# Optimization experiments

Hardware: AMD Instinct MI355X
Metric: run time of the kernel (lower is better)

## Reference

```python
import jax, jax.numpy as jnp
import numpy as np

HEADS = 16
DIM_HEAD = 64
SCALE = float(np.sqrt(DIM_HEAD))  # NOTE: original code MULTIPLIES by sqrt(dim_head)


def setup_inputs() -> dict:
    key = jax.random.key(0)
    k1, k2, k3, k4 = jax.random.split(key, 4)
    dim = 1024
    b, n = 2, 2048
    s = 1.0 / np.sqrt(dim)
    return {
        "x": jax.random.normal(k1, (b, n, dim), dtype=jnp.float32),
        "w_q": jax.random.normal(k2, (dim, HEADS * DIM_HEAD), dtype=jnp.float32) * s,
        "w_vk": jax.random.normal(k3, (dim, HEADS * DIM_HEAD * 2), dtype=jnp.float32) * s,
        "w_out": jax.random.normal(k4, (HEADS * DIM_HEAD, dim), dtype=jnp.float32) * s,
    }


def reference(x, w_q, w_vk, w_out):
    b, n, _ = x.shape
    h, d = HEADS, DIM_HEAD
    context = x  # context=None, kv_include_self=False
    q = (x @ w_q).reshape(b, n, h, d).transpose(0, 2, 1, 3)          # b h n d
    kv = context @ w_vk                                              # b n 2hd
    k, v = jnp.split(kv, 2, axis=-1)                                 # chunk order: k first, v second
    k = k.reshape(b, n, h, d).transpose(0, 2, 1, 3)
    v = v.reshape(b, n, h, d).transpose(0, 2, 1, 3)
    dots = jnp.einsum('bhid,bhjd->bhij', q, k) * SCALE               # faithful: multiply by sqrt(d)
    attn = jax.nn.softmax(dots, axis=-1)                             # dropout p=0 -> identity
    out = jnp.einsum('bhij,bhjd->bhid', attn, v)
    out = out.transpose(0, 2, 1, 3).reshape(b, n, h * d)
    return out @ w_out
```

## Files before the change

kernel.cpp:

```cpp
#include <hip/hip_runtime.h>

typedef _Float16 half4 __attribute__((ext_vector_type(4)));
typedef _Float16 half8 __attribute__((ext_vector_type(8)));
typedef float f32x4 __attribute__((ext_vector_type(4)));

#define MFMA_F16K32(a, b, c) __builtin_amdgcn_mfma_f32_16x16x32_f16(a, b, c, 0, 0, 0)
#define MFMA_F16K16(a, b, c) __builtin_amdgcn_mfma_f32_16x16x16f16(a, b, c, 0, 0, 0)
#define EXP2F(x) __builtin_amdgcn_exp2f(x)

constexpr int NSEQ = 2048, DIM = 1024;
constexpr int MROWS = 4096;
constexpr float QSCALE = 11.5415603271f;

__device__ __forceinline__ void ld_lds16(void* lds, const void* g) {
  __builtin_amdgcn_global_load_lds(
      (const __attribute__((address_space(1))) void*)g,
      (__attribute__((address_space(3))) void*)lds, 16, 0, 0);
}

__global__ __launch_bounds__(256) void prep(
    const float* __restrict__ w_q, const float* __restrict__ w_vk,
    const float* __restrict__ w_out, const float* __restrict__ x,
    _Float16* __restrict__ WT, _Float16* __restrict__ WoT,
    _Float16* __restrict__ xf) {
  const int bid = blockIdx.x;
  const int t = threadIdx.x;
  if (bid >= 1024) {
    const size_t i = ((size_t)(bid - 1024) * 256 + t) * 8;
    float4 a = *(const float4*)(x + i), b2 = *(const float4*)(x + i + 4);
    float v[8] = {a.x, a.y, a.z, a.w, b2.x, b2.y, b2.z, b2.w};
    half8 h;
#pragma unroll
    for (int j = 0; j < 8; ++j) h[j] = (_Float16)v[j];
    *(half8*)(xf + i) = h;
    return;
  }
  __shared__ float T[64][65];
  const int bx = bid & 63, k0 = (bid >> 6) * 64;
  const float* src;
  int srcN, n0, dstrow, mode;
  float scale;
  if (bx < 16) {
    src = w_q; srcN = 1024; n0 = bx * 64; dstrow = n0; scale = QSCALE; mode = 0;
  } else if (bx < 48) {
    src = w_vk; srcN = 2048; n0 = (bx - 16) * 64; dstrow = 1024 + n0;
    scale = 1.0f; mode = 0;
  } else {
    src = w_out; srcN = 1024; n0 = (bx - 48) * 64; dstrow = n0;
    scale = 1.0f; mode = 1;
  }
  {
    const int r = t >> 2, c4 = (t & 3) * 16;
    const float* s = src + (size_t)(k0 + r) * srcN + n0 + c4;
    float4 v0 = ((const float4*)s)[0], v1 = ((const float4*)s)[1],
           v2 = ((const float4*)s)[2], v3 = ((const float4*)s)[3];
    *(float4*)&T[r][c4 + 0] = v0;  *(float4*)&T[r][c4 + 4] = v1;
    *(float4*)&T[r][c4 + 8] = v2;  *(float4*)&T[r][c4 + 12] = v3;
  }
  __syncthreads();
  const int rn = t >> 2, kc = (t & 3) * 16;
  half8 hv[2];
#pragma unroll
  for (int half = 0; half < 2; ++half)
#pragma unroll
    for (int j = 0; j < 8; ++j)
      hv[half][j] = (_Float16)(T[kc + half * 8 + j][rn] * scale);
  _Float16* d = ((mode == 0) ? WT + (size_t)(dstrow + rn) * 1024
                             : WoT + (size_t)(n0 + rn) * 1024) + k0 + kc;
  *(half8*)d = hv[0]; *(half8*)(d + 8) = hv[1];
}

__global__ __launch_bounds__(256, 3) void proj6(
    const _Float16* __restrict__ xf, const _Float16* __restrict__ WT,
    _Float16* __restrict__ qb, _Float16* __restrict__ kb,
    _Float16* __restrict__ VT) {
  __shared__ __align__(16) char smem[32768];
  const int t = threadIdx.x;
  const int lane = t & 63, wave = t >> 6, quad = lane >> 4, lq = lane & 15;
  const int bn = blockIdx.x * 128, bm = blockIdx.y * 128;
  const int kind = bn >> 10;
  const int wm = (wave >> 1) * 64, wn = (wave & 1) * 64;

  const int srow = lane >> 2;
  const int schk = (lane & 3) ^ (srow & 3);
  const _Float16* xg = xf + (size_t)(bm + wave * 32 + srow) * DIM + schk * 8;
  const _Float16* bg = WT + (size_t)(bn + wave * 32 + srow) * DIM + schk * 8;
  const int wb = wave * 2048;

  auto issue = [&](char* buf, int k0) {
    ld_lds16(buf + wb,                xg + k0);
    ld_lds16(buf + wb + 1024,         xg + k0 + 16 * DIM);
    ld_lds16(buf + 8192 + wb,         bg + k0);
    ld_lds16(buf + 8192 + wb + 1024,  bg + k0 + 16 * DIM);
  };

  const int swz = (quad ^ (lq & 3)) * 8;

  f32x4 acc[4][4];
#pragma unroll
  for (int i = 0; i < 4; ++i)
#pragma unroll
    for (int j = 0; j < 4; ++j) acc[i][j] = (f32x4){0.f, 0.f, 0.f, 0.f};

  char* bufA = smem;
  char* bufB = smem + 16384;
  issue(bufA, 0);
  for (int k0 = 0; k0 < DIM; k0 += 32) {
    char* cur = ((k0 >> 5) & 1) ? bufB : bufA;
    char* nxt = ((k0 >> 5) & 1) ? bufA : bufB;
    __syncthreads();
    if (k0 + 32 < DIM) issue(nxt, k0 + 32);
    const _Float16* Xs = (const _Float16*)cur;
    const _Float16* Bs = (const _Float16*)(cur + 8192);
    half8 ah[4];
#pragma unroll
    for (int i = 0; i < 4; ++i)
      ah[i] = *(const half8*)&Xs[(wm + i * 16 + lq) * 32 + swz];
#pragma unroll
    for (int j = 0; j < 4; ++j) {
      half8 bf = *(const half8*)&Bs[(wn + j * 16 + lq) * 32 + swz];
#pragma unroll
      for (int i = 0; i < 4; ++i) acc[i][j] = MFMA_F16K32(ah[i], bf, acc[i][j]);
    }
  }

  if (kind == 2) {
#pragma unroll
    for (int i = 0; i < 4; ++i)
#pragma unroll
      for (int j = 0; j < 4; ++j) {
        const int c = (bn - 2048) + wn + j * 16 + lq;
        const int row0 = bm + wm + i * 16 + quad * 4;
        const int b = row0 >> 11, n = row0 & 2047;
        const int h = c >> 6, d = c & 63;
        half4 o;
#pragma unroll
        for (int r = 0; r < 4; ++r) o[r] = (_Float16)acc[i][j][r];
        *(half4*)(VT + ((size_t)(b * 16 + h) * 64 + d) * 2048 + n) = o;
      }
  } else {
    _Float16* D = (kind == 0) ? qb : kb;
    const int cb = bn & 1023;
#pragma unroll
    for (int i = 0; i < 4; ++i)
#pragma unroll
      for (int j = 0; j < 4; ++j) {
        const int col = cb + wn + j * 16 + lq;
#pragma unroll
        for (int r = 0; r < 4; ++r) {
          const int row = bm + wm + i * 16 + quad * 4 + r;
          D[(size_t)row * 1024 + col] = (_Float16)acc[i][j][r];
        }
      }
  }
}

__global__ __launch_bounds__(256, 2) void attn7(
    const _Float16* __restrict__ qb, const _Float16* __restrict__ kb,
    const _Float16* __restrict__ vT, _Float16* __restrict__ ho) {
  __shared__ __align__(16) char smem[65536];
  const int t = threadIdx.x;
  const int lane = t & 63, wave = t >> 6, quad = lane >> 4, lq = lane & 15;
  const int i0 = blockIdx.x * 128;
  const int bh = blockIdx.y, b = bh >> 4, head = bh & 15;
  const size_t rowbase = (size_t)b * NSEQ;

  half8 qf[2][2];
#pragma unroll
  for (int qt = 0; qt < 2; ++qt) {
    const _Float16* qp =
        qb + (rowbase + i0 + wave * 32 + qt * 16 + lq) * DIM + head * 64 + quad * 8;
    qf[qt][0] = *(const half8*)qp;
    qf[qt][1] = *(const half8*)(qp + 32);
  }

  f32x4 o[2][4];
#pragma unroll
  for (int qt = 0; qt < 2; ++qt)
#pragma unroll
    for (int dt = 0; dt < 4; ++dt) o[qt][dt] = (f32x4){0.f, 0.f, 0.f, 0.f};
  float mrun[2] = {-3.0e38f, -3.0e38f};
  float lrun[2] = {0.f, 0.f};

  const int srow = lane >> 3, schk = (lane & 7) ^ srow;
  const _Float16* kg =
      kb + (rowbase + wave * 32 + srow) * DIM + head * 64 + schk * 8;
  int vco[4];
#pragma unroll
  for (int is = 0; is < 4; ++is)
    vco[is] = ((lane & 15) ^ (is * 4 + (lane >> 4))) * 8;
  const _Float16* vg = vT + ((size_t)bh * 64 + wave * 16 + (lane >> 4)) * NSEQ;

  auto issue = [&](char* buf, int j0) {
#pragma unroll
    for (int is = 0; is < 4; ++is) {
      ld_lds16(buf + wave * 4096 + is * 1024,
               kg + ((size_t)j0 + is * 8) * DIM);
      ld_lds16(buf + 16384 + (wave * 16 + is * 4) * 256,
               vg + (size_t)is * 4 * NSEQ + j0 + vco[is]);
    }
  };

  const int swzK0 = (quad ^ (lq & 7)) * 8;
  const int swzK1 = ((quad + 4) ^ (lq & 7)) * 8;

  char* bufA = smem;
  char* bufB = smem + 32768;
  issue(bufA, 0);

  for (int j0 = 0; j0 < NSEQ; j0 += 128) {
    char* cur = ((j0 >> 7) & 1) ? bufB : bufA;
    char* nxt = ((j0 >> 7) & 1) ? bufA : bufB;
    __syncthreads();
    if (j0 + 128 < NSEQ) issue(nxt, j0 + 128);
    const _Float16* Khs = (const _Float16*)cur;
    const _Float16* Vts = (const _Float16*)(cur + 16384);

#pragma unroll
    for (int jh = 0; jh < 2; ++jh) {
      f32x4 s[2][4];
#pragma unroll
      for (int nt = 0; nt < 4; ++nt) {
        const int roff = (jh * 64 + nt * 16 + lq) * 64;
        half8 k0f = *(const half8*)&Khs[roff + swzK0];
        half8 k1f = *(const half8*)&Khs[roff + swzK1];
#pragma unroll
        for (int qt = 0; qt < 2; ++qt) {
          f32x4 sv = (f32x4){0.f, 0.f, 0.f, 0.f};
          sv = MFMA_F16K32(k0f, qf[qt][0], sv);
          sv = MFMA_F16K32(k1f, qf[qt][1], sv);
          s[qt][nt] = sv;
        }
      }
      half4 pb[2][4];
#pragma unroll
      for (int qt = 0; qt < 2; ++qt) {
        float mx = s[qt][0][0];
#pragma unroll
        for (int nt = 0; nt < 4; ++nt)
#pragma unroll
          for (int r = 0; r < 4; ++r) mx = fmaxf(mx, s[qt][nt][r]);
        mx = fmaxf(mx, __shfl_xor(mx, 16));
        mx = fmaxf(mx, __shfl_xor(mx, 32));
        const float mn = fmaxf(mrun[qt], mx);
        const float alpha = EXP2F(mrun[qt] - mn);
        mrun[qt] = mn;
        float rs = 0.f;
#pragma unroll
        for (int nt = 0; nt < 4; ++nt)
#pragma unroll
          for (int r = 0; r < 4; ++r) {
            float p = EXP2F(s[qt][nt][r] - mn);
            rs += p;
            pb[qt][nt][r] = (_Float16)p;
          }
        rs += __shfl_xor(rs, 16);
        rs += __shfl_xor(rs, 32);
        lrun[qt] = lrun[qt] * alpha + rs;
#pragma unroll
        for (int dt = 0; dt < 4; ++dt) o[qt][dt] *= alpha;
      }
#pragma unroll
      for (int dt = 0; dt < 4; ++dt) {
        const int vrow = (dt * 16 + lq) * 128;
#pragma unroll
        for (int nt = 0; nt < 4; ++nt) {
          const int ntj = jh * 4 + nt;
          const int voff =
              vrow + ((2 * ntj + (quad >> 1)) ^ lq) * 8 + (quad & 1) * 4;
          half4 va = *(const half4*)&Vts[voff];
          o[0][dt] = MFMA_F16K16(va, pb[0][nt], o[0][dt]);
          o[1][dt] = MFMA_F16K16(va, pb[1][nt], o[1][dt]);
        }
      }
    }
  }

  _Float16* Ots = (_Float16*)smem;
  __syncthreads();
#pragma unroll
  for (int qt = 0; qt < 2; ++qt) {
    const float inv = 1.0f / lrun[qt];
#pragma unroll
    for (int dt = 0; dt < 4; ++dt)
#pragma unroll
      for (int r = 0; r < 4; ++r)
        Ots[(wave * 32 + qt * 16 + lq) * 80 + dt * 16 + quad * 4 + r] =
            (_Float16)(o[qt][dt][r] * inv);
  }
  __syncthreads();
  {
    const int row = t >> 1, hf = t & 1;
    const _Float16* src = &Ots[row * 80 + hf * 32];
    half8 o0 = ((const half8*)src)[0], o1 = ((const half8*)src)[1],
          o2 = ((const half8*)src)[2], o3 = ((const half8*)src)[3];
    _Float16* dst = ho + (rowbase + i0 + row) * DIM + head * 64 + hf * 32;
    ((half8*)dst)[0] = o0; ((half8*)dst)[1] = o1;
    ((half8*)dst)[2] = o2; ((half8*)dst)[3] = o3;
  }
}

__global__ __launch_bounds__(256, 4) void gemm_out(
    const _Float16* __restrict__ A, const _Float16* __restrict__ BT,
    float* __restrict__ C) {
  __shared__ __align__(16) char smem[24576];
  const int t = threadIdx.x;
  const int lane = t & 63, wave = t >> 6, quad = lane >> 4, lq = lane & 15;
  const int bn = blockIdx.x * 128, bm = blockIdx.y * 64;
  const int wm = (wave >> 1) * 32, wn = (wave & 1) * 64;

  const int bco = (lane & 7) ^ (lane >> 3);
  const int brow = 2 * (lane >> 3) + (bco >> 2);
  const int bcc = bco & 3;
  const _Float16* ag = A + (size_t)(bm + wave * 16 + brow) * DIM + bcc * 8;
  const _Float16* bg = BT + (size_t)(bn + wave * 32 + brow) * DIM + bcc * 8;
  const int swzB = ((((lq & 1) << 2) | quad) ^ ((lq >> 1) & 7)) * 8;

  auto issue = [&](char* buf, int k0) {
    ld_lds16(buf + wave * 1024,               ag + k0);
    ld_lds16(buf + 4096 + wave * 2048,        bg + k0);
    ld_lds16(buf + 4096 + wave * 2048 + 1024, bg + k0 + 16 * DIM);
  };

  f32x4 acc[2][4];
#pragma unroll
  for (int i = 0; i < 2; ++i)
#pragma unroll
    for (int j = 0; j < 4; ++j) acc[i][j] = (f32x4){0.f, 0.f, 0.f, 0.f};

  char* bufA = smem;
  char* bufB = smem + 12288;
  issue(bufA, 0);
  for (int k0 = 0; k0 < DIM; k0 += 32) {
    char* cur = ((k0 >> 5) & 1) ? bufB : bufA;
    char* nxt = ((k0 >> 5) & 1) ? bufA : bufB;
    __syncthreads();
    if (k0 + 32 < DIM) issue(nxt, k0 + 32);
    const _Float16* Ahs = (const _Float16*)cur;
    const _Float16* Bhs = (const _Float16*)(cur + 4096);
    half8 ah[2];
#pragma unroll
    for (int i = 0; i < 2; ++i) {
      const int row = wm + i * 16 + lq;
      ah[i] = *(const half8*)&Ahs[(row >> 1) * 64 + swzB];
    }
#pragma unroll
    for (int j = 0; j < 4; ++j) {
      const int row = wn + j * 16 + lq;
      half8 bf = *(const half8*)&Bhs[(row >> 1) * 64 + swzB];
#pragma unroll
      for (int i = 0; i < 2; ++i) acc[i][j] = MFMA_F16K32(ah[i], bf, acc[i][j]);
    }
  }
#pragma unroll
  for (int i = 0; i < 2; ++i)
#pragma unroll
    for (int j = 0; j < 4; ++j) {
      const int col = bn + wn + j * 16 + lq;
#pragma unroll
      for (int r = 0; r < 4; ++r) {
        const int row = bm + wm + i * 16 + quad * 4 + r;
        C[(size_t)row * 1024 + col] = acc[i][j][r];
      }
    }
}

extern "C" void kernel_launch(void* const* d_in, const int* in_sizes, int n_in,
                              void* d_out, int out_size, void* d_ws,
                              size_t ws_size, hipStream_t stream) {
  const float* x     = (const float*)d_in[0];
  const float* w_q   = (const float*)d_in[1];
  const float* w_vk  = (const float*)d_in[2];
  const float* w_out = (const float*)d_in[3];
  float* out = (float*)d_out;

  char* w = (char*)d_ws;
  _Float16* wT  = (_Float16*)(w);
  _Float16* woT = (_Float16*)(w + (6ull << 20));
  _Float16* qbb = (_Float16*)(w + (8ull << 20));
  _Float16* kbb = (_Float16*)(w + (16ull << 20));
  _Float16* vTb = (_Float16*)(w + (24ull << 20));
  _Float16* hob = (_Float16*)(w + (32ull << 20));
  _Float16* xfb = (_Float16*)(w + (40ull << 20));

  dim3 blk(256);
  prep<<<dim3(3072), blk, 0, stream>>>(w_q, w_vk, w_out, x, wT, woT, xfb);
  proj6<<<dim3(24, 32), blk, 0, stream>>>(xfb, wT, qbb, kbb, vTb);
  attn7<<<dim3(16, 32), blk, 0, stream>>>(qbb, kbb, vTb, hob);
  gemm_out<<<dim3(8, 64), blk, 0, stream>>>(hob, woT, out);
}
```

Measured before the change: 187.5 us.

## Split attention block across eight waves of sixteen query rows each

The attention kernel now runs 512-thread blocks, so each of eight waves owns 16 query rows instead of four waves owning 32. The K/V tile loads are redistributed across the waves with a matching V swizzle, and the output write-back is spread over all 512 threads. Each wave now handles the full 128-key tile in one pass instead of two 64-key halves. Probabilities are converted with packed fp16 conversion, and MFMA sections are wrapped in s_setprio. The aim is more waves to hide latency and less per-wave softmax bookkeeping, but the (512,4) launch bound sharply caps VGPRs per thread and may cause spills, while 64KB LDS per block still limits how many blocks fit on a CU.

```diff
diff --git a/kernel.cpp b/kernel.cpp
--- a/kernel.cpp
+++ b/kernel.cpp
@@ -2,11 +2,13 @@
 
 typedef _Float16 half4 __attribute__((ext_vector_type(4)));
 typedef _Float16 half8 __attribute__((ext_vector_type(8)));
+typedef _Float16 h2pk __attribute__((ext_vector_type(2)));
 typedef float f32x4 __attribute__((ext_vector_type(4)));
 
 #define MFMA_F16K32(a, b, c) __builtin_amdgcn_mfma_f32_16x16x32_f16(a, b, c, 0, 0, 0)
 #define MFMA_F16K16(a, b, c) __builtin_amdgcn_mfma_f32_16x16x16f16(a, b, c, 0, 0, 0)
 #define EXP2F(x) __builtin_amdgcn_exp2f(x)
+#define CVT_PK(a, b) __builtin_bit_cast(h2pk, __builtin_amdgcn_cvt_pkrtz(a, b))
 
 constexpr int NSEQ = 2048, DIM = 1024;
 constexpr int MROWS = 4096;
@@ -155,7 +157,7 @@
   }
 }
 
-__global__ __launch_bounds__(256, 2) void attn7(
+__global__ __launch_bounds__(512, 4) void attn7(
     const _Float16* __restrict__ qb, const _Float16* __restrict__ kb,
     const _Float16* __restrict__ vT, _Float16* __restrict__ ho) {
   __shared__ __align__(16) char smem[65536];
@@ -165,38 +167,36 @@
   const int bh = blockIdx.y, b = bh >> 4, head = bh & 15;
   const size_t rowbase = (size_t)b * NSEQ;
 
-  half8 qf[2][2];
-#pragma unroll
-  for (int qt = 0; qt < 2; ++qt) {
+  half8 qf0, qf1;
+  {
     const _Float16* qp =
-        qb + (rowbase + i0 + wave * 32 + qt * 16 + lq) * DIM + head * 64 + quad * 8;
-    qf[qt][0] = *(const half8*)qp;
-    qf[qt][1] = *(const half8*)(qp + 32);
-  }
-
-  f32x4 o[2][4];
-#pragma unroll
-  for (int qt = 0; qt < 2; ++qt)
-#pragma unroll
-    for (int dt = 0; dt < 4; ++dt) o[qt][dt] = (f32x4){0.f, 0.f, 0.f, 0.f};
-  float mrun[2] = {-3.0e38f, -3.0e38f};
-  float lrun[2] = {0.f, 0.f};
+        qb + (rowbase + i0 + wave * 16 + lq) * DIM + head * 64 + quad * 8;
+    qf0 = *(const half8*)qp;
+    qf1 = *(const half8*)(qp + 32);
+  }
+
+  f32x4 o[4];
+#pragma unroll
+  for (int dt = 0; dt < 4; ++dt) o[dt] = (f32x4){0.f, 0.f, 0.f, 0.f};
+  float mrun = -3.0e38f;
+  float lrun = 0.f;
 
   const int srow = lane >> 3, schk = (lane & 7) ^ srow;
   const _Float16* kg =
-      kb + (rowbase + wave * 32 + srow) * DIM + head * 64 + schk * 8;
-  int vco[4];
-#pragma unroll
-  for (int is = 0; is < 4; ++is)
-    vco[is] = ((lane & 15) ^ (is * 4 + (lane >> 4))) * 8;
-  const _Float16* vg = vT + ((size_t)bh * 64 + wave * 16 + (lane >> 4)) * NSEQ;
+      kb + (rowbase + wave * 16 + srow) * DIM + head * 64 + schk * 8;
+  const int vr = lane >> 4;
+  int vco[2];
+#pragma unroll
+  for (int is = 0; is < 2; ++is)
+    vco[is] = ((lane & 15) ^ ((wave & 1) * 8 + is * 4 + vr)) * 8;
+  const _Float16* vg = vT + ((size_t)bh * 64 + wave * 8 + vr) * NSEQ;
 
   auto issue = [&](char* buf, int j0) {
 #pragma unroll
-    for (int is = 0; is < 4; ++is) {
-      ld_lds16(buf + wave * 4096 + is * 1024,
+    for (int is = 0; is < 2; ++is) {
+      ld_lds16(buf + wave * 2048 + is * 1024,
                kg + ((size_t)j0 + is * 8) * DIM);
-      ld_lds16(buf + 16384 + (wave * 16 + is * 4) * 256,
+      ld_lds16(buf + 16384 + (wave * 8 + is * 4) * 256,
                vg + (size_t)is * 4 * NSEQ + j0 + vco[is]);
     }
   };
@@ -216,87 +216,88 @@
     const _Float16* Khs = (const _Float16*)cur;
     const _Float16* Vts = (const _Float16*)(cur + 16384);
 
-#pragma unroll
-    for (int jh = 0; jh < 2; ++jh) {
-      f32x4 s[2][4];
-#pragma unroll
-      for (int nt = 0; nt < 4; ++nt) {
-        const int roff = (jh * 64 + nt * 16 + lq) * 64;
-        half8 k0f = *(const half8*)&Khs[roff + swzK0];
-        half8 k1f = *(const half8*)&Khs[roff + swzK1];
-#pragma unroll
-        for (int qt = 0; qt < 2; ++qt) {
-          f32x4 sv = (f32x4){0.f, 0.f, 0.f, 0.f};
-          sv = MFMA_F16K32(k0f, qf[qt][0], sv);
-          sv = MFMA_F16K32(k1f, qf[qt][1], sv);
-          s[qt][nt] = sv;
-        }
+    f32x4 s[8];
+    __builtin_amdgcn_s_setprio(1);
+#pragma unroll
+    for (int nt = 0; nt < 8; ++nt) {
+      const int roff = (nt * 16 + lq) * 64;
+      half8 k0f = *(const half8*)&Khs[roff + swzK0];
+      half8 k1f = *(const half8*)&Khs[roff + swzK1];
+      f32x4 sv = (f32x4){0.f, 0.f, 0.f, 0.f};
+      sv = MFMA_F16K32(k0f, qf0, sv);
+      sv = MFMA_F16K32(k1f, qf1, sv);
+      s[nt] = sv;
+    }
+    __builtin_amdgcn_s_setprio(0);
+
+    float mx;
+    {
+      float m0 = fmaxf(fmaxf(s[0][0], s[0][1]), fmaxf(s[0][2], s[0][3]));
+      float m1 = fmaxf(fmaxf(s[1][0], s[1][1]), fmaxf(s[1][2], s[1][3]));
+      float m2 = fmaxf(fmaxf(s[2][0], s[2][1]), fmaxf(s[2][2], s[2][3]));
+      float m3 = fmaxf(fmaxf(s[3][0], s[3][1]), fmaxf(s[3][2], s[3][3]));
+      float m4 = fmaxf(fmaxf(s[4][0], s[4][1]), fmaxf(s[4][2], s[4][3]));
+      float m5 = fmaxf(fmaxf(s[5][0], s[5][1]), fmaxf(s[5][2], s[5][3]));
+      float m6 = fmaxf(fmaxf(s[6][0], s[6][1]), fmaxf(s[6][2], s[6][3]));
+      float m7 = fmaxf(fmaxf(s[7][0], s[7][1]), fmaxf(s[7][2], s[7][3]));
+      mx = fmaxf(fmaxf(fmaxf(m0, m1), fmaxf(m2, m3)),
+                 fmaxf(fmaxf(m4, m5), fmaxf(m6, m7)));
+    }
+    mx = fmaxf(mx, __shfl_xor(mx, 16));
+    mx = fmaxf(mx, __shfl_xor(mx, 32));
+    const float mn = fmaxf(mrun, mx);
+    const float alpha = EXP2F(mrun - mn);
+    mrun = mn;
+    float rs = 0.f;
+    half4 pb[8];
+#pragma unroll
+    for (int nt = 0; nt < 8; ++nt) {
+      float p0 = EXP2F(s[nt][0] - mn), p1 = EXP2F(s[nt][1] - mn);
+      float p2 = EXP2F(s[nt][2] - mn), p3 = EXP2F(s[nt][3] - mn);
+      rs += (p0 + p1) + (p2 + p3);
+      h2pk lo = CVT_PK(p0, p1);
+      h2pk hi = CVT_PK(p2, p3);
+      pb[nt] = (half4){lo[0], lo[1], hi[0], hi[1]};
+    }
+    rs += __shfl_xor(rs, 16);
+    rs += __shfl_xor(rs, 32);
+    lrun = lrun * alpha + rs;
+#pragma unroll
+    for (int dt = 0; dt < 4; ++dt) o[dt] *= alpha;
+
+    __builtin_amdgcn_s_setprio(1);
+#pragma unroll
+    for (int dt = 0; dt < 4; ++dt) {
+      const int vrow = (dt * 16 + lq) * 128;
+#pragma unroll
+      for (int ntj = 0; ntj < 8; ++ntj) {
+        const int voff =
+            vrow + ((2 * ntj + (quad >> 1)) ^ lq) * 8 + (quad & 1) * 4;
+        half4 va = *(const half4*)&Vts[voff];
+        o[dt] = MFMA_F16K16(va, pb[ntj], o[dt]);
       }
-      half4 pb[2][4];
-#pragma unroll
-      for (int qt = 0; qt < 2; ++qt) {
-        float mx = s[qt][0][0];
-#pragma unroll
-        for (int nt = 0; nt < 4; ++nt)
-#pragma unroll
-          for (int r = 0; r < 4; ++r) mx = fmaxf(mx, s[qt][nt][r]);
-        mx = fmaxf(mx, __shfl_xor(mx, 16));
-        mx = fmaxf(mx, __shfl_xor(mx, 32));
-        const float mn = fmaxf(mrun[qt], mx);
-        const float alpha = EXP2F(mrun[qt] - mn);
-        mrun[qt] = mn;
-        float rs = 0.f;
-#pragma unroll
-        for (int nt = 0; nt < 4; ++nt)
-#pragma unroll
-          for (int r = 0; r < 4; ++r) {
-            float p = EXP2F(s[qt][nt][r] - mn);
-            rs += p;
-            pb[qt][nt][r] = (_Float16)p;
-          }
-        rs += __shfl_xor(rs, 16);
-        rs += __shfl_xor(rs, 32);
-        lrun[qt] = lrun[qt] * alpha + rs;
-#pragma unroll
-        for (int dt = 0; dt < 4; ++dt) o[qt][dt] *= alpha;
-      }
-#pragma unroll
-      for (int dt = 0; dt < 4; ++dt) {
-        const int vrow = (dt * 16 + lq) * 128;
-#pragma unroll
-        for (int nt = 0; nt < 4; ++nt) {
-          const int ntj = jh * 4 + nt;
-          const int voff =
-              vrow + ((2 * ntj + (quad >> 1)) ^ lq) * 8 + (quad & 1) * 4;
-          half4 va = *(const half4*)&Vts[voff];
-          o[0][dt] = MFMA_F16K16(va, pb[0][nt], o[0][dt]);
-          o[1][dt] = MFMA_F16K16(va, pb[1][nt], o[1][dt]);
-        }
-      }
-    }
+    }
+    __builtin_amdgcn_s_setprio(0);
   }
 
   _Float16* Ots = (_Float16*)smem;
   __syncthreads();
-#pragma unroll
-  for (int qt = 0; qt < 2; ++qt) {
-    const float inv = 1.0f / lrun[qt];
+  {
+    const float inv = 1.0f / lrun;
 #pragma unroll
     for (int dt = 0; dt < 4; ++dt)
 #pragma unroll
       for (int r = 0; r < 4; ++r)
-        Ots[(wave * 32 + qt * 16 + lq) * 80 + dt * 16 + quad * 4 + r] =
-            (_Float16)(o[qt][dt][r] * inv);
+        Ots[(wave * 16 + lq) * 80 + dt * 16 + quad * 4 + r] =
+            (_Float16)(o[dt][r] * inv);
   }
   __syncthreads();
   {
-    const int row = t >> 1, hf = t & 1;
-    const _Float16* src = &Ots[row * 80 + hf * 32];
-    half8 o0 = ((const half8*)src)[0], o1 = ((const half8*)src)[1],
-          o2 = ((const half8*)src)[2], o3 = ((const half8*)src)[3];
-    _Float16* dst = ho + (rowbase + i0 + row) * DIM + head * 64 + hf * 32;
+    const int row = t >> 2, seg = t & 3;
+    const _Float16* src = &Ots[row * 80 + seg * 16];
+    half8 o0 = ((const half8*)src)[0], o1 = ((const half8*)src)[1];
+    _Float16* dst = ho + (rowbase + i0 + row) * DIM + head * 64 + seg * 16;
     ((half8*)dst)[0] = o0; ((half8*)dst)[1] = o1;
-    ((half8*)dst)[2] = o2; ((half8*)dst)[3] = o3;
   }
 }
 
@@ -386,6 +387,6 @@
   dim3 blk(256);
   prep<<<dim3(3072), blk, 0, stream>>>(w_q, w_vk, w_out, x, wT, woT, xfb);
   proj6<<<dim3(24, 32), blk, 0, stream>>>(xfb, wT, qbb, kbb, vTb);
-  attn7<<<dim3(16, 32), blk, 0, stream>>>(qbb, kbb, vTb, hob);
+  attn7<<<dim3(16, 32), dim3(512), 0, stream>>>(qbb, kbb, vTb, hob);
   gemm_out<<<dim3(8, 64), blk, 0, stream>>>(hob, woT, out);
 }
```

After: 192.1 us. 2.4% more time.

## Split attention KV sequence across two wave groups and merge partial softmax states

Applied to the files above, without the earlier changes.

The attention kernel now uses 512 threads per block in two groups of four waves. Each group handles alternating 64-key tiles of the same 128 query rows, and at the end group 1 dumps its partial O, max and sum to LDS for group 0 to merge. The aim is more waves per CU for latency hiding and MFMA/exp overlap; it also adds s_setprio around the MFMA sections and packed f16 conversion. The costs are a final merge pass, per-wave register pressure under launch_bounds(512,4), and smaller per-group tiles.

```diff
diff --git a/kernel.cpp b/kernel.cpp
--- a/kernel.cpp
+++ b/kernel.cpp
@@ -2,14 +2,15 @@
 
 typedef _Float16 half4 __attribute__((ext_vector_type(4)));
 typedef _Float16 half8 __attribute__((ext_vector_type(8)));
+typedef _Float16 h2pk __attribute__((ext_vector_type(2)));
 typedef float f32x4 __attribute__((ext_vector_type(4)));
 
 #define MFMA_F16K32(a, b, c) __builtin_amdgcn_mfma_f32_16x16x32_f16(a, b, c, 0, 0, 0)
 #define MFMA_F16K16(a, b, c) __builtin_amdgcn_mfma_f32_16x16x16f16(a, b, c, 0, 0, 0)
 #define EXP2F(x) __builtin_amdgcn_exp2f(x)
+#define CVT_PK(a, b) __builtin_bit_cast(h2pk, __builtin_amdgcn_cvt_pkrtz(a, b))
 
 constexpr int NSEQ = 2048, DIM = 1024;
-constexpr int MROWS = 4096;
 constexpr float QSCALE = 11.5415603271f;
 
 __device__ __forceinline__ void ld_lds16(void* lds, const void* g) {
@@ -155,12 +156,13 @@
   }
 }
 
-__global__ __launch_bounds__(256, 2) void attn7(
+__global__ __launch_bounds__(512, 4) void attn8(
     const _Float16* __restrict__ qb, const _Float16* __restrict__ kb,
     const _Float16* __restrict__ vT, _Float16* __restrict__ ho) {
   __shared__ __align__(16) char smem[65536];
   const int t = threadIdx.x;
   const int lane = t & 63, wave = t >> 6, quad = lane >> 4, lq = lane & 15;
+  const int group = wave >> 2, wq = wave & 3;
   const int i0 = blockIdx.x * 128;
   const int bh = blockIdx.y, b = bh >> 4, head = bh & 15;
   const size_t rowbase = (size_t)b * NSEQ;
@@ -169,7 +171,7 @@
 #pragma unroll
   for (int qt = 0; qt < 2; ++qt) {
     const _Float16* qp =
-        qb + (rowbase + i0 + wave * 32 + qt * 16 + lq) * DIM + head * 64 + quad * 8;
+        qb + (rowbase + i0 + wq * 32 + qt * 16 + lq) * DIM + head * 64 + quad * 8;
     qf[qt][0] = *(const half8*)qp;
     qf[qt][1] = *(const half8*)(qp + 32);
   }
@@ -183,120 +185,140 @@
   float lrun[2] = {0.f, 0.f};
 
   const int srow = lane >> 3, schk = (lane & 7) ^ srow;
-  const _Float16* kg =
-      kb + (rowbase + wave * 32 + srow) * DIM + head * 64 + schk * 8;
-  int vco[4];
-#pragma unroll
-  for (int is = 0; is < 4; ++is)
-    vco[is] = ((lane & 15) ^ (is * 4 + (lane >> 4))) * 8;
-  const _Float16* vg = vT + ((size_t)bh * 64 + wave * 16 + (lane >> 4)) * NSEQ;
-
-  auto issue = [&](char* buf, int j0) {
-#pragma unroll
-    for (int is = 0; is < 4; ++is) {
-      ld_lds16(buf + wave * 4096 + is * 1024,
-               kg + ((size_t)j0 + is * 8) * DIM);
-      ld_lds16(buf + 16384 + (wave * 16 + is * 4) * 256,
-               vg + (size_t)is * 4 * NSEQ + j0 + vco[is]);
-    }
+  const _Float16* kgp =
+      kb + (rowbase + wq * 16 + srow) * DIM + head * 64 + schk * 8;
+  const _Float16* vgp =
+      vT + ((size_t)bh * 64 + wq * 16 + srow) * 2048 + schk * 8;
+
+  auto issue = [&](int bsel, int j) {
+    char* kd = smem + (group * 2 + bsel) * 8192 + wq * 2048;
+    char* vd = kd + 32768;
+    ld_lds16(kd,        kgp + (size_t)j * DIM);
+    ld_lds16(kd + 1024, kgp + (size_t)(j + 8) * DIM);
+    ld_lds16(vd,        vgp + j);
+    ld_lds16(vd + 1024, vgp + 8 * 2048 + j);
   };
 
   const int swzK0 = (quad ^ (lq & 7)) * 8;
   const int swzK1 = ((quad + 4) ^ (lq & 7)) * 8;
 
-  char* bufA = smem;
-  char* bufB = smem + 32768;
-  issue(bufA, 0);
-
-  for (int j0 = 0; j0 < NSEQ; j0 += 128) {
-    char* cur = ((j0 >> 7) & 1) ? bufB : bufA;
-    char* nxt = ((j0 >> 7) & 1) ? bufA : bufB;
+  issue(0, group * 64);
+
+  for (int p = 0; p < 16; ++p) {
+    const int cur = p & 1;
     __syncthreads();
-    if (j0 + 128 < NSEQ) issue(nxt, j0 + 128);
-    const _Float16* Khs = (const _Float16*)cur;
-    const _Float16* Vts = (const _Float16*)(cur + 16384);
-
-#pragma unroll
-    for (int jh = 0; jh < 2; ++jh) {
-      f32x4 s[2][4];
+    if (p < 15) issue(cur ^ 1, (2 * p + group) * 64 + 128);
+    const _Float16* Khs = (const _Float16*)(smem + (group * 2 + cur) * 8192);
+    const _Float16* Vts = (const _Float16*)(smem + 32768 + (group * 2 + cur) * 8192);
+
+    f32x4 s[2][4];
+    __builtin_amdgcn_s_setprio(1);
+#pragma unroll
+    for (int nt = 0; nt < 4; ++nt) {
+      const int roff = (nt * 16 + lq) * 64;
+      half8 k0f = *(const half8*)&Khs[roff + swzK0];
+      half8 k1f = *(const half8*)&Khs[roff + swzK1];
+#pragma unroll
+      for (int qt = 0; qt < 2; ++qt) {
+        f32x4 sv = (f32x4){0.f, 0.f, 0.f, 0.f};
+        sv = MFMA_F16K32(k0f, qf[qt][0], sv);
+        sv = MFMA_F16K32(k1f, qf[qt][1], sv);
+        s[qt][nt] = sv;
+      }
+    }
+    __builtin_amdgcn_s_setprio(0);
+
+    half4 pbv[2][4];
+#pragma unroll
+    for (int qt = 0; qt < 2; ++qt) {
+      float m0 = fmaxf(fmaxf(s[qt][0][0], s[qt][0][1]),
+                       fmaxf(s[qt][0][2], s[qt][0][3]));
+      float m1 = fmaxf(fmaxf(s[qt][1][0], s[qt][1][1]),
+                       fmaxf(s[qt][1][2], s[qt][1][3]));
+      float m2 = fmaxf(fmaxf(s[qt][2][0], s[qt][2][1]),
+                       fmaxf(s[qt][2][2], s[qt][2][3]));
+      float m3 = fmaxf(fmaxf(s[qt][3][0], s[qt][3][1]),
+                       fmaxf(s[qt][3][2], s[qt][3][3]));
+      float mx = fmaxf(fmaxf(m0, m1), fmaxf(m2, m3));
+      mx = fmaxf(mx, __shfl_xor(mx, 16));
+      mx = fmaxf(mx, __shfl_xor(mx, 32));
+      const float mn = fmaxf(mrun[qt], mx);
+      const float alpha = EXP2F(mrun[qt] - mn);
+      mrun[qt] = mn;
+      float rs = 0.f;
 #pragma unroll
       for (int nt = 0; nt < 4; ++nt) {
-        const int roff = (jh * 64 + nt * 16 + lq) * 64;
-        half8 k0f = *(const half8*)&Khs[roff + swzK0];
-        half8 k1f = *(const half8*)&Khs[roff + swzK1];
-#pragma unroll
-        for (int qt = 0; qt < 2; ++qt) {
-          f32x4 sv = (f32x4){0.f, 0.f, 0.f, 0.f};
-          sv = MFMA_F16K32(k0f, qf[qt][0], sv);
-          sv = MFMA_F16K32(k1f, qf[qt][1], sv);
-          s[qt][nt] = sv;
+        float p0 = EXP2F(s[qt][nt][0] - mn), p1 = EXP2F(s[qt][nt][1] - mn);
+        float p2 = EXP2F(s[qt][nt][2] - mn), p3 = EXP2F(s[qt][nt][3] - mn);
+        rs += (p0 + p1) + (p2 + p3);
+        h2pk lo = CVT_PK(p0, p1);
+        h2pk hi = CVT_PK(p2, p3);
+        pbv[qt][nt] = (half4){lo[0], lo[1], hi[0], hi[1]};
+      }
+      rs += __shfl_xor(rs, 16);
+      rs += __shfl_xor(rs, 32);
+      lrun[qt] = lrun[qt] * alpha + rs;
+#pragma unroll
+      for (int dt = 0; dt < 4; ++dt) o[qt][dt] *= alpha;
+    }
+
+    __builtin_amdgcn_s_setprio(1);
+#pragma unroll
+    for (int dt = 0; dt < 4; ++dt) {
+      const int vrow = (dt * 16 + lq) * 64;
+#pragma unroll
+      for (int ntj = 0; ntj < 4; ++ntj) {
+        const int voff =
+            vrow + (((2 * ntj + (quad >> 1)) ^ (lq & 7)) * 8) + (quad & 1) * 4;
+        half4 va = *(const half4*)&Vts[voff];
+        o[0][dt] = MFMA_F16K16(va, pbv[0][ntj], o[0][dt]);
+        o[1][dt] = MFMA_F16K16(va, pbv[1][ntj], o[1][dt]);
+      }
+    }
+    __builtin_amdgcn_s_setprio(0);
+  }
+
+  float* dump = (float*)smem;
+  __syncthreads();
+  if (group == 1) {
+    float* D = dump + wq * 2304 + lane * 36;
+#pragma unroll
+    for (int qt = 0; qt < 2; ++qt)
+#pragma unroll
+      for (int dt = 0; dt < 4; ++dt)
+        *(f32x4*)(D + (qt * 4 + dt) * 4) = o[qt][dt];
+    D[32] = mrun[0]; D[33] = lrun[0]; D[34] = mrun[1]; D[35] = lrun[1];
+  }
+  __syncthreads();
+  _Float16* Ots = (_Float16*)(smem + 40960);
+  if (group == 0) {
+    const float* D = dump + wq * 2304 + lane * 36;
+#pragma unroll
+    for (int qt = 0; qt < 2; ++qt) {
+      const float m2 = D[32 + qt * 2], l2 = D[33 + qt * 2];
+      const float mM = fmaxf(mrun[qt], m2);
+      const float f1 = EXP2F(mrun[qt] - mM);
+      const float f2 = EXP2F(m2 - mM);
+      const float inv = 1.0f / (lrun[qt] * f1 + l2 * f2);
+#pragma unroll
+      for (int dt = 0; dt < 4; ++dt) {
+        f32x4 o2 = *(const f32x4*)(D + (qt * 4 + dt) * 4);
+#pragma unroll
+        for (int r = 0; r < 4; ++r) {
+          const float val = (o[qt][dt][r] * f1 + o2[r] * f2) * inv;
+          Ots[(wq * 32 + qt * 16 + lq) * 80 + dt * 16 + quad * 4 + r] =
+              (_Float16)val;
         }
       }
-      half4 pb[2][4];
-#pragma unroll
-      for (int qt = 0; qt < 2; ++qt) {
-        float mx = s[qt][0][0];
-#pragma unroll
-        for (int nt = 0; nt < 4; ++nt)
-#pragma unroll
-          for (int r = 0; r < 4; ++r) mx = fmaxf(mx, s[qt][nt][r]);
-        mx = fmaxf(mx, __shfl_xor(mx, 16));
-        mx = fmaxf(mx, __shfl_xor(mx, 32));
-        const float mn = fmaxf(mrun[qt], mx);
-        const float alpha = EXP2F(mrun[qt] - mn);
-        mrun[qt] = mn;
-        float rs = 0.f;
-#pragma unroll
-        for (int nt = 0; nt < 4; ++nt)
-#pragma unroll
-          for (int r = 0; r < 4; ++r) {
-            float p = EXP2F(s[qt][nt][r] - mn);
-            rs += p;
-            pb[qt][nt][r] = (_Float16)p;
-          }
-        rs += __shfl_xor(rs, 16);
-        rs += __shfl_xor(rs, 32);
-        lrun[qt] = lrun[qt] * alpha + rs;
-#pragma unroll
-        for (int dt = 0; dt < 4; ++dt) o[qt][dt] *= alpha;
-      }
-#pragma unroll
-      for (int dt = 0; dt < 4; ++dt) {
-        const int vrow = (dt * 16 + lq) * 128;
-#pragma unroll
-        for (int nt = 0; nt < 4; ++nt) {
-          const int ntj = jh * 4 + nt;
-          const int voff =
-              vrow + ((2 * ntj + (quad >> 1)) ^ lq) * 8 + (quad & 1) * 4;
-          half4 va = *(const half4*)&Vts[voff];
-          o[0][dt] = MFMA_F16K16(va, pb[0][nt], o[0][dt]);
-          o[1][dt] = MFMA_F16K16(va, pb[1][nt], o[1][dt]);
-        }
-      }
-    }
-  }
-
-  _Float16* Ots = (_Float16*)smem;
-  __syncthreads();
-#pragma unroll
-  for (int qt = 0; qt < 2; ++qt) {
-    const float inv = 1.0f / lrun[qt];
-#pragma unroll
-    for (int dt = 0; dt < 4; ++dt)
-#pragma unroll
-      for (int r = 0; r < 4; ++r)
-        Ots[(wave * 32 + qt * 16 + lq) * 80 + dt * 16 + quad * 4 + r] =
-            (_Float16)(o[qt][dt][r] * inv);
+    }
   }
   __syncthreads();
   {
-    const int row = t >> 1, hf = t & 1;
-    const _Float16* src = &Ots[row * 80 + hf * 32];
-    half8 o0 = ((const half8*)src)[0], o1 = ((const half8*)src)[1],
-          o2 = ((const half8*)src)[2], o3 = ((const half8*)src)[3];
-    _Float16* dst = ho + (rowbase + i0 + row) * DIM + head * 64 + hf * 32;
+    const int row = t >> 2, seg = t & 3;
+    const _Float16* src = &Ots[row * 80 + seg * 16];
+    half8 o0 = ((const half8*)src)[0], o1 = ((const half8*)src)[1];
+    _Float16* dst = ho + (rowbase + i0 + row) * DIM + head * 64 + seg * 16;
     ((half8*)dst)[0] = o0; ((half8*)dst)[1] = o1;
-    ((half8*)dst)[2] = o2; ((half8*)dst)[3] = o3;
   }
 }
 
@@ -386,6 +408,6 @@
   dim3 blk(256);
   prep<<<dim3(3072), blk, 0, stream>>>(w_q, w_vk, w_out, x, wT, woT, xfb);
   proj6<<<dim3(24, 32), blk, 0, stream>>>(xfb, wT, qbb, kbb, vTb);
-  attn7<<<dim3(16, 32), blk, 0, stream>>>(qbb, kbb, vTb, hob);
+  attn8<<<dim3(16, 32), dim3(512), 0, stream>>>(qbb, kbb, vTb, hob);
   gemm_out<<<dim3(8, 64), blk, 0, stream>>>(hob, woT, out);
 }
```

Result: no change. 189.1 us (+0.9%).
